# Kernel tuning notes

Measured on AMD Instinct MI355X. Metric: run time of the kernel, lower is better.

The kernel has to match this reference:

```python
import jax, jax.numpy as jnp
import numpy as np

N = 50000      # nodes
E = 600000     # edges
D_IN = 128
D_HID = 128
D_OUT = 64
BN_EPS = 1e-5


def _linear(key, fan_in, fan_out):
    s = 1.0 / np.sqrt(fan_in)
    kw, kb = jax.random.split(key)
    W = jax.random.uniform(kw, (fan_in, fan_out), jnp.float32, -s, s)
    b = jax.random.uniform(kb, (fan_out,), jnp.float32, -s, s)
    return W, b


def setup_inputs() -> dict:
    key = jax.random.key(0)
    ks = jax.random.split(key, 6)
    x = jax.random.normal(ks[0], (N, D_IN), jnp.float32)
    edge_index = jax.random.randint(ks[1], (2, E), 0, N, dtype=jnp.int64)
    W1, b1 = _linear(ks[2], D_IN, D_HID)
    W2, b2 = _linear(ks[3], D_HID, D_HID)
    W3, b3 = _linear(ks[4], D_HID, D_OUT)
    g1 = jnp.ones((D_HID,), jnp.float32); be1 = jnp.zeros((D_HID,), jnp.float32)
    g2 = jnp.ones((D_HID,), jnp.float32); be2 = jnp.zeros((D_HID,), jnp.float32)
    return {"x": x, "edge_index": edge_index,
            "W1": W1, "b1": b1, "g1": g1, "be1": be1,
            "W2": W2, "b2": b2, "g2": g2, "be2": be2,
            "W3": W3, "b3": b3}


def _gin_conv(x, src, dst, W, b):
    # GIN aggregation: h_i = (1+eps)*x_i + sum_{j->i} x_j, eps=0, then linear
    agg = jax.ops.segment_sum(x[src], dst, num_segments=N)  # [N, d]
    return (agg + x) @ W + b


def _bn(x, gamma, beta):
    # BatchNorm1d in training mode: batch statistics over nodes
    m = x.mean(axis=0)
    v = x.var(axis=0)
    return (x - m) * jax.lax.rsqrt(v + BN_EPS) * gamma + beta


def reference(x, edge_index, W1, b1, g1, be1, W2, b2, g2, be2, W3, b3):
    src, dst = edge_index[0], edge_index[1]
    h = jax.nn.relu(_bn(_gin_conv(x, src, dst, W1, b1), g1, be1))
    h = jax.nn.relu(_bn(_gin_conv(h, src, dst, W2, b2), g2, be2))
    h = _gin_conv(h, src, dst, W3, b3)
    return jax.nn.log_softmax(h, axis=-1)
```

## Files before the change

kernel.cpp:

```cpp
#include <hip/hip_runtime.h>

#define BN_EPS 1e-5f

typedef __attribute__((ext_vector_type(8))) __bf16 bf16x8;
typedef __attribute__((ext_vector_type(4))) float f32x4;

__device__ __forceinline__ unsigned short f2bf(float f) {
    unsigned int u = __float_as_uint(f);
    u = (u + 0x7fffu + ((u >> 16) & 1u)) >> 16;
    return (unsigned short)u;
}
__device__ __forceinline__ float bfLo(unsigned int w) { return __uint_as_float(w << 16); }
__device__ __forceinline__ float bfHi(unsigned int w) { return __uint_as_float(w & 0xffff0000u); }


__global__ void hist_kernel(const int* __restrict__ dst, int* __restrict__ deg, int E) {
    int e = blockIdx.x * blockDim.x + threadIdx.x;
    if (e < E) atomicAdd(&deg[dst[e]], 1);
}

__global__ void scan_block(const int* __restrict__ deg, int* __restrict__ incl,
                           int* __restrict__ bsum, int N) {
    __shared__ int s[256];
    int i = blockIdx.x * 256 + threadIdx.x;
    int v = (i < N) ? deg[i] : 0;
    s[threadIdx.x] = v;
    __syncthreads();
#pragma unroll
    for (int off = 1; off < 256; off <<= 1) {
        int t = (threadIdx.x >= off) ? s[threadIdx.x - off] : 0;
        __syncthreads();
        s[threadIdx.x] += t;
        __syncthreads();
    }
    if (i < N) incl[i] = s[threadIdx.x];
    if (threadIdx.x == 255) bsum[blockIdx.x] = s[255];
}

__global__ void scan_top(int* __restrict__ bsum, int nb) {
    __shared__ int s[256];
    int v = (threadIdx.x < nb) ? bsum[threadIdx.x] : 0;
    s[threadIdx.x] = v;
    __syncthreads();
#pragma unroll
    for (int off = 1; off < 256; off <<= 1) {
        int t = (threadIdx.x >= off) ? s[threadIdx.x - off] : 0;
        __syncthreads();
        s[threadIdx.x] += t;
        __syncthreads();
    }
    if (threadIdx.x < nb) bsum[threadIdx.x] = s[threadIdx.x] - v;
}

__global__ void finalize_rowptr(const int* __restrict__ deg, const int* __restrict__ incl,
                                const int* __restrict__ boff, int* __restrict__ rowptr,
                                int* __restrict__ pos, int N, int E) {
    int i = blockIdx.x * 256 + threadIdx.x;
    if (i < N) {
        int r = incl[i] - deg[i] + boff[i >> 8];
        rowptr[i] = r;
        pos[i] = r;
    }
    if (i == 0) rowptr[N] = E;
}

__global__ void fill_kernel(const int* __restrict__ src, const int* __restrict__ dst,
                            int* __restrict__ pos, int* __restrict__ col, int E) {
    int e = blockIdx.x * blockDim.x + threadIdx.x;
    if (e < E) {
        int slot = atomicAdd(&pos[dst[e]], 1);
        col[slot] = src[e];
    }
}

__global__ void convert_and_prep(const float* __restrict__ x, unsigned short* __restrict__ hb,
                                 int total4,
                                 const float* __restrict__ W1, const float* __restrict__ W2,
                                 const float* __restrict__ W3,
                                 unsigned short* __restrict__ w1s, unsigned short* __restrict__ w2s,
                                 unsigned short* __restrict__ w3s) {
    int tid0 = blockIdx.x * blockDim.x + threadIdx.x;
    if (tid0 < 40960) {
        int idx = tid0;
        const float* W; unsigned short* O; int NOUT;
        if (idx < 16384)      { W = W1; O = w1s; NOUT = 128; }
        else if (idx < 32768) { W = W2; O = w2s; NOUT = 128; idx -= 16384; }
        else                  { W = W3; O = w3s; NOUT = 64;  idx -= 32768; }
        int j = idx & 7;
        int l = (idx >> 3) & 63;
        int q = (idx >> 9) & 3;
        int ct = idx >> 11;
        int k = q * 32 + ((l >> 4) & 3) * 8 + j;
        int c = ct * 16 + (l & 15);
        O[idx] = f2bf(W[(size_t)k * NOUT + c]);
    }
    int stride = gridDim.x * blockDim.x;
    for (int i = tid0; i < total4; i += stride) {
        float4 v = reinterpret_cast<const float4*>(x)[i];
        ushort4 o;
        o.x = f2bf(v.x); o.y = f2bf(v.y); o.z = f2bf(v.z); o.w = f2bf(v.w);
        reinterpret_cast<ushort4*>(hb)[i] = o;
    }
}

__global__ void gather_agg_bf(const unsigned short* __restrict__ h,
                              const int* __restrict__ rowptr, const int* __restrict__ col,
                              unsigned short* __restrict__ agg, int N) {
    int t = blockIdx.x * blockDim.x + threadIdx.x;
    int node = t >> 4;
    if (node >= N) return;
    int part = (t & 15) * 8;
    const int beg = rowptr[node], end = rowptr[node + 1];

    float acc[8];
    {
        uint4 sv = *reinterpret_cast<const uint4*>(h + (size_t)node * 128 + part);
        acc[0] = bfLo(sv.x); acc[1] = bfHi(sv.x);
        acc[2] = bfLo(sv.y); acc[3] = bfHi(sv.y);
        acc[4] = bfLo(sv.z); acc[5] = bfHi(sv.z);
        acc[6] = bfLo(sv.w); acc[7] = bfHi(sv.w);
    }
    int e = beg;
    for (; e + 1 < end; e += 2) {
        int s0 = col[e], s1 = col[e + 1];
        uint4 v0 = *reinterpret_cast<const uint4*>(h + (size_t)s0 * 128 + part);
        uint4 v1 = *reinterpret_cast<const uint4*>(h + (size_t)s1 * 128 + part);
        acc[0] += bfLo(v0.x) + bfLo(v1.x); acc[1] += bfHi(v0.x) + bfHi(v1.x);
        acc[2] += bfLo(v0.y) + bfLo(v1.y); acc[3] += bfHi(v0.y) + bfHi(v1.y);
        acc[4] += bfLo(v0.z) + bfLo(v1.z); acc[5] += bfHi(v0.z) + bfHi(v1.z);
        acc[6] += bfLo(v0.w) + bfLo(v1.w); acc[7] += bfHi(v0.w) + bfHi(v1.w);
    }
    if (e < end) {
        uint4 v0 = *reinterpret_cast<const uint4*>(h + (size_t)col[e] * 128 + part);
        acc[0] += bfLo(v0.x); acc[1] += bfHi(v0.x);
        acc[2] += bfLo(v0.y); acc[3] += bfHi(v0.y);
        acc[4] += bfLo(v0.z); acc[5] += bfHi(v0.z);
        acc[6] += bfLo(v0.w); acc[7] += bfHi(v0.w);
    }
    uint4 o;
    o.x = (unsigned int)f2bf(acc[0]) | ((unsigned int)f2bf(acc[1]) << 16);
    o.y = (unsigned int)f2bf(acc[2]) | ((unsigned int)f2bf(acc[3]) << 16);
    o.z = (unsigned int)f2bf(acc[4]) | ((unsigned int)f2bf(acc[5]) << 16);
    o.w = (unsigned int)f2bf(acc[6]) | ((unsigned int)f2bf(acc[7]) << 16);
    *reinterpret_cast<uint4*>(agg + (size_t)node * 128 + part) = o;
}

__global__ __launch_bounds__(256) void gemm128_stats(const unsigned short* __restrict__ A,
                                                     const unsigned short* __restrict__ Wsw,
                                                     const float* __restrict__ bias,
                                                     float* __restrict__ out,
                                                     float* __restrict__ sumsPad,
                                                     float* __restrict__ sqsPad, int N) {
    __shared__ float red[2][4][128];
    const int lane = threadIdx.x & 63;
    const int w = threadIdx.x >> 6;
    const int r0 = blockIdx.x * 64 + w * 16;
    int arow = r0 + (lane & 15);
    if (arow >= N) arow = N - 1;
    const int kb = lane >> 4;
    const unsigned short* ap = A + (size_t)arow * 128 + kb * 8;

    bf16x8 a[4];
#pragma unroll
    for (int q = 0; q < 4; ++q) a[q] = *reinterpret_cast<const bf16x8*>(ap + q * 32);

    f32x4 acc[8];
#pragma unroll
    for (int ct = 0; ct < 8; ++ct) acc[ct] = (f32x4){0.f, 0.f, 0.f, 0.f};

    const bf16x8* wp = reinterpret_cast<const bf16x8*>(Wsw) + lane;
#pragma unroll
    for (int ct = 0; ct < 8; ++ct)
#pragma unroll
        for (int q = 0; q < 4; ++q)
            acc[ct] = __builtin_amdgcn_mfma_f32_16x16x32_bf16(a[q], wp[(ct * 4 + q) * 64],
                                                              acc[ct], 0, 0, 0);

    const int crow0 = r0 + (lane >> 4) * 4;
    const int ccol = lane & 15;
#pragma unroll
    for (int ct = 0; ct < 8; ++ct) {
        int c = ct * 16 + ccol;
        float bv = bias[c];
        float s = 0.f, qq = 0.f;
#pragma unroll
        for (int j = 0; j < 4; ++j) {
            int r = crow0 + j;
            if (r < N) {
                float o = acc[ct][j] + bv;
                out[(size_t)r * 128 + c] = o;
                s += o; qq += o * o;
            }
        }
        s += __shfl_xor(s, 16); s += __shfl_xor(s, 32);
        qq += __shfl_xor(qq, 16); qq += __shfl_xor(qq, 32);
        if (lane < 16) { red[0][w][c] = s; red[1][w][c] = qq; }
    }
    __syncthreads();
    int tid = threadIdx.x;
    if (tid < 128) {
        float S = red[0][0][tid] + red[0][1][tid] + red[0][2][tid] + red[0][3][tid];
        atomicAdd(&sumsPad[tid * 16], S);
    } else {
        int c = tid - 128;
        float Q = red[1][0][c] + red[1][1][c] + red[1][2][c] + red[1][3][c];
        atomicAdd(&sqsPad[c * 16], Q);
    }
}

__global__ __launch_bounds__(256) void gemm64_lsm(const unsigned short* __restrict__ A,
                                                  const unsigned short* __restrict__ Wsw,
                                                  const float* __restrict__ bias,
                                                  float* __restrict__ out, int N) {
    const int lane = threadIdx.x & 63;
    const int w = threadIdx.x >> 6;
    const int r0 = blockIdx.x * 64 + w * 16;
    int arow = r0 + (lane & 15);
    if (arow >= N) arow = N - 1;
    const int kb = lane >> 4;
    const unsigned short* ap = A + (size_t)arow * 128 + kb * 8;

    bf16x8 a[4];
#pragma unroll
    for (int q = 0; q < 4; ++q) a[q] = *reinterpret_cast<const bf16x8*>(ap + q * 32);

    f32x4 acc[4];
#pragma unroll
    for (int ct = 0; ct < 4; ++ct) acc[ct] = (f32x4){0.f, 0.f, 0.f, 0.f};

    const bf16x8* wp = reinterpret_cast<const bf16x8*>(Wsw) + lane;
#pragma unroll
    for (int ct = 0; ct < 4; ++ct)
#pragma unroll
        for (int q = 0; q < 4; ++q)
            acc[ct] = __builtin_amdgcn_mfma_f32_16x16x32_bf16(a[q], wp[(ct * 4 + q) * 64],
                                                              acc[ct], 0, 0, 0);

    const int crow0 = r0 + (lane >> 4) * 4;
    const int ccol = lane & 15;
    float bv[4];
#pragma unroll
    for (int ct = 0; ct < 4; ++ct) bv[ct] = bias[ct * 16 + ccol];

#pragma unroll
    for (int j = 0; j < 4; ++j) {
        float o0 = acc[0][j] + bv[0], o1 = acc[1][j] + bv[1];
        float o2 = acc[2][j] + bv[2], o3 = acc[3][j] + bv[3];
        float m = fmaxf(fmaxf(o0, o1), fmaxf(o2, o3));
#pragma unroll
        for (int off = 1; off < 16; off <<= 1) m = fmaxf(m, __shfl_xor(m, off));
        float s = __expf(o0 - m) + __expf(o1 - m) + __expf(o2 - m) + __expf(o3 - m);
#pragma unroll
        for (int off = 1; off < 16; off <<= 1) s += __shfl_xor(s, off);
        float ml = m + __logf(s);
        int r = crow0 + j;
        if (r < N) {
            float* op = out + (size_t)r * 64 + ccol;
            op[0]  = o0 - ml;
            op[16] = o1 - ml;
            op[32] = o2 - ml;
            op[48] = o3 - ml;
        }
    }
}

__global__ void bn_relu_bf16(const float* __restrict__ t, const float* __restrict__ sumsPad,
                             const float* __restrict__ sqsPad, const float* __restrict__ g,
                             const float* __restrict__ be, unsigned short* __restrict__ h,
                             int total4, float invN) {
    const int idx0 = blockIdx.x * blockDim.x + threadIdx.x;
    const int stride = gridDim.x * blockDim.x;
    const int col = (idx0 * 4) & 127;
    float a4[4], c4[4];
#pragma unroll
    for (int k = 0; k < 4; ++k) {
        int c = col + k;
        float m = sumsPad[c * 16] * invN;
        float v = sqsPad[c * 16] * invN - m * m;
        float ai = g[c] * rsqrtf(v + BN_EPS);
        a4[k] = ai;
        c4[k] = be[c] - m * ai;
    }
    for (int idx = idx0; idx < total4; idx += stride) {
        float4 v = reinterpret_cast<const float4*>(t)[idx];
        ushort4 o;
        o.x = f2bf(fmaxf(fmaf(v.x, a4[0], c4[0]), 0.f));
        o.y = f2bf(fmaxf(fmaf(v.y, a4[1], c4[1]), 0.f));
        o.z = f2bf(fmaxf(fmaf(v.z, a4[2], c4[2]), 0.f));
        o.w = f2bf(fmaxf(fmaf(v.w, a4[3], c4[3]), 0.f));
        reinterpret_cast<ushort4*>(h)[idx] = o;
    }
}

extern "C" void kernel_launch(void* const* d_in, const int* in_sizes, int n_in,
                              void* d_out, int out_size, void* d_ws, size_t ws_size,
                              hipStream_t stream) {
    const float* x   = (const float*)d_in[0];
    const int*   ei  = (const int*)d_in[1];
    const float* W1  = (const float*)d_in[2];
    const float* b1  = (const float*)d_in[3];
    const float* g1  = (const float*)d_in[4];
    const float* be1 = (const float*)d_in[5];
    const float* W2  = (const float*)d_in[6];
    const float* b2  = (const float*)d_in[7];
    const float* g2  = (const float*)d_in[8];
    const float* be2 = (const float*)d_in[9];
    const float* W3  = (const float*)d_in[10];
    const float* b3  = (const float*)d_in[11];

    const int N = in_sizes[0] / 128;
    const int E = in_sizes[1] / 2;
    const int* src = ei;
    const int* dst = ei + E;

    float* f1           = (float*)d_ws;
    unsigned short* hb  = (unsigned short*)(f1 + (size_t)N * 128);
    unsigned short* agb = hb + (size_t)N * 128;
    unsigned short* w1s = agb + (size_t)N * 128;
    unsigned short* w2s = w1s + 16384;
    unsigned short* w3s = w2s + 16384;
    float* statsPad = (float*)(w3s + 8192);
    float* sums1 = statsPad;
    float* sqs1  = statsPad + 2048;
    float* sums2 = statsPad + 4096;
    float* sqs2  = statsPad + 6144;
    int* deg    = (int*)(statsPad + 8192);
    int* pos    = deg + N;
    int* rowptr = pos + N;
    int* bsum   = rowptr + N + 1;
    int* colidx = bsum + 256;

    const int nChunks = (N + 255) / 256;
    const int eBlocks = (E + 255) / 256;
    const int gemmBlocks = (N + 63) / 64;
    const int gatherBlocks = (N * 16 + 255) / 256;
    const int total4 = N * 128 / 4;

    hipMemsetAsync(statsPad, 0, 8192 * sizeof(float) + (size_t)N * sizeof(int), stream);

    convert_and_prep<<<2048, 256, 0, stream>>>(x, hb, total4, W1, W2, W3, w1s, w2s, w3s);
    hist_kernel<<<eBlocks, 256, 0, stream>>>(dst, deg, E);
    scan_block<<<nChunks, 256, 0, stream>>>(deg, pos, bsum, N);
    scan_top<<<1, 256, 0, stream>>>(bsum, nChunks);
    finalize_rowptr<<<nChunks, 256, 0, stream>>>(deg, pos, bsum, rowptr, pos, N, E);
    fill_kernel<<<eBlocks, 256, 0, stream>>>(src, dst, pos, colidx, E);

    gather_agg_bf<<<gatherBlocks, 256, 0, stream>>>(hb, rowptr, colidx, agb, N);
    gemm128_stats<<<gemmBlocks, 256, 0, stream>>>(agb, w1s, b1, f1, sums1, sqs1, N);
    bn_relu_bf16<<<2048, 256, 0, stream>>>(f1, sums1, sqs1, g1, be1, hb, total4, 1.0f / N);

    gather_agg_bf<<<gatherBlocks, 256, 0, stream>>>(hb, rowptr, colidx, agb, N);
    gemm128_stats<<<gemmBlocks, 256, 0, stream>>>(agb, w2s, b2, f1, sums2, sqs2, N);
    bn_relu_bf16<<<2048, 256, 0, stream>>>(f1, sums2, sqs2, g2, be2, hb, total4, 1.0f / N);

    gather_agg_bf<<<gatherBlocks, 256, 0, stream>>>(hb, rowptr, colidx, agb, N);
    gemm64_lsm<<<gemmBlocks, 256, 0, stream>>>(agb, w3s, b3, (float*)d_out, N);
}
```

Baseline: 258.3 us.

## Fuse BN+ReLU into gather, store GEMM output as bf16, degree-sort nodes

The GEMM epilogue now writes pre-BN activations as bf16 instead of fp32, and the standalone bn_relu pass is removed. BN scale/shift and ReLU are instead applied on the fly to every gathered neighbor row inside a new gather_bn_agg kernel. Nodes are also bucketed by degree via a histogram and permutation so that the 16-lane groups in a wavefront handle nodes of similar degree, which reduces divergence. The trade-off is redundant BN arithmetic per edge, plus rounding to bf16 before the normalization is applied.

```diff
diff --git a/kernel.cpp b/kernel.cpp
--- a/kernel.cpp
+++ b/kernel.cpp
@@ -20,12 +20,15 @@
 }
 
 __global__ void scan_block(const int* __restrict__ deg, int* __restrict__ incl,
-                           int* __restrict__ bsum, int N) {
+                           int* __restrict__ bsum, int* __restrict__ bhist, int N) {
     __shared__ int s[256];
+    __shared__ int bh[64];
     int i = blockIdx.x * 256 + threadIdx.x;
     int v = (i < N) ? deg[i] : 0;
     s[threadIdx.x] = v;
+    if (threadIdx.x < 64) bh[threadIdx.x] = 0;
     __syncthreads();
+    if (i < N) atomicAdd(&bh[v < 63 ? v : 63], 1);
 #pragma unroll
     for (int off = 1; off < 256; off <<= 1) {
         int t = (threadIdx.x >= off) ? s[threadIdx.x - off] : 0;
@@ -35,9 +38,11 @@
     }
     if (i < N) incl[i] = s[threadIdx.x];
     if (threadIdx.x == 255) bsum[blockIdx.x] = s[255];
-}
-
-__global__ void scan_top(int* __restrict__ bsum, int nb) {
+    if (threadIdx.x < 64 && bh[threadIdx.x] > 0) atomicAdd(&bhist[threadIdx.x], bh[threadIdx.x]);
+}
+
+__global__ void scan_top(int* __restrict__ bsum, int nb,
+                         const int* __restrict__ bhist, int* __restrict__ bpos) {
     __shared__ int s[256];
     int v = (threadIdx.x < nb) ? bsum[threadIdx.x] : 0;
     s[threadIdx.x] = v;
@@ -50,16 +55,30 @@
         __syncthreads();
     }
     if (threadIdx.x < nb) bsum[threadIdx.x] = s[threadIdx.x] - v;
+    if (threadIdx.x < 64) {
+        int bv = bhist[threadIdx.x];
+        int inc = bv;
+#pragma unroll
+        for (int off = 1; off < 64; off <<= 1) {
+            int t = __shfl_up(inc, off);
+            if ((threadIdx.x & 63) >= off) inc += t;
+        }
+        bpos[threadIdx.x] = inc - bv;
+    }
 }
 
 __global__ void finalize_rowptr(const int* __restrict__ deg, const int* __restrict__ incl,
                                 const int* __restrict__ boff, int* __restrict__ rowptr,
-                                int* __restrict__ pos, int N, int E) {
+                                int* __restrict__ pos, int* __restrict__ bpos,
+                                int* __restrict__ perm, int N, int E) {
     int i = blockIdx.x * 256 + threadIdx.x;
     if (i < N) {
-        int r = incl[i] - deg[i] + boff[i >> 8];
+        int d = deg[i];
+        int r = incl[i] - d + boff[i >> 8];
         rowptr[i] = r;
         pos[i] = r;
+        int slot = atomicAdd(&bpos[d < 63 ? d : 63], 1);
+        perm[slot] = i;
     }
     if (i == 0) rowptr[N] = E;
 }
@@ -105,10 +124,12 @@
 
 __global__ void gather_agg_bf(const unsigned short* __restrict__ h,
                               const int* __restrict__ rowptr, const int* __restrict__ col,
+                              const int* __restrict__ perm,
                               unsigned short* __restrict__ agg, int N) {
     int t = blockIdx.x * blockDim.x + threadIdx.x;
-    int node = t >> 4;
-    if (node >= N) return;
+    int ni = t >> 4;
+    if (ni >= N) return;
+    int node = perm[ni];
     int part = (t & 15) * 8;
     const int beg = rowptr[node], end = rowptr[node + 1];
 
@@ -145,10 +166,65 @@
     *reinterpret_cast<uint4*>(agg + (size_t)node * 128 + part) = o;
 }
 
+__global__ void gather_bn_agg(const unsigned short* __restrict__ raw,
+                              const float* __restrict__ sumsPad, const float* __restrict__ sqsPad,
+                              const float* __restrict__ g, const float* __restrict__ be,
+                              const int* __restrict__ rowptr, const int* __restrict__ col,
+                              const int* __restrict__ perm,
+                              unsigned short* __restrict__ agg, int N, float invN) {
+    int t = blockIdx.x * blockDim.x + threadIdx.x;
+    int ni = t >> 4;
+    if (ni >= N) return;
+    int node = perm[ni];
+    int part = (t & 15) * 8;
+    float a8[8], c8[8];
+#pragma unroll
+    for (int k = 0; k < 8; ++k) {
+        int c = part + k;
+        float m = sumsPad[c * 16] * invN;
+        float v = sqsPad[c * 16] * invN - m * m;
+        float ai = g[c] * rsqrtf(v + BN_EPS);
+        a8[k] = ai;
+        c8[k] = be[c] - m * ai;
+    }
+    const int beg = rowptr[node], end = rowptr[node + 1];
+    float acc[8];
+    {
+        uint4 sv = *reinterpret_cast<const uint4*>(raw + (size_t)node * 128 + part);
+        float e0 = bfLo(sv.x), e1 = bfHi(sv.x), e2 = bfLo(sv.y), e3 = bfHi(sv.y);
+        float e4 = bfLo(sv.z), e5 = bfHi(sv.z), e6 = bfLo(sv.w), e7 = bfHi(sv.w);
+        acc[0] = fmaxf(fmaf(e0, a8[0], c8[0]), 0.f);
+        acc[1] = fmaxf(fmaf(e1, a8[1], c8[1]), 0.f);
+        acc[2] = fmaxf(fmaf(e2, a8[2], c8[2]), 0.f);
+        acc[3] = fmaxf(fmaf(e3, a8[3], c8[3]), 0.f);
+        acc[4] = fmaxf(fmaf(e4, a8[4], c8[4]), 0.f);
+        acc[5] = fmaxf(fmaf(e5, a8[5], c8[5]), 0.f);
+        acc[6] = fmaxf(fmaf(e6, a8[6], c8[6]), 0.f);
+        acc[7] = fmaxf(fmaf(e7, a8[7], c8[7]), 0.f);
+    }
+    for (int e = beg; e < end; ++e) {
+        uint4 v0 = *reinterpret_cast<const uint4*>(raw + (size_t)col[e] * 128 + part);
+        acc[0] += fmaxf(fmaf(bfLo(v0.x), a8[0], c8[0]), 0.f);
+        acc[1] += fmaxf(fmaf(bfHi(v0.x), a8[1], c8[1]), 0.f);
+        acc[2] += fmaxf(fmaf(bfLo(v0.y), a8[2], c8[2]), 0.f);
+        acc[3] += fmaxf(fmaf(bfHi(v0.y), a8[3], c8[3]), 0.f);
+        acc[4] += fmaxf(fmaf(bfLo(v0.z), a8[4], c8[4]), 0.f);
+        acc[5] += fmaxf(fmaf(bfHi(v0.z), a8[5], c8[5]), 0.f);
+        acc[6] += fmaxf(fmaf(bfLo(v0.w), a8[6], c8[6]), 0.f);
+        acc[7] += fmaxf(fmaf(bfHi(v0.w), a8[7], c8[7]), 0.f);
+    }
+    uint4 o;
+    o.x = (unsigned int)f2bf(acc[0]) | ((unsigned int)f2bf(acc[1]) << 16);
+    o.y = (unsigned int)f2bf(acc[2]) | ((unsigned int)f2bf(acc[3]) << 16);
+    o.z = (unsigned int)f2bf(acc[4]) | ((unsigned int)f2bf(acc[5]) << 16);
+    o.w = (unsigned int)f2bf(acc[6]) | ((unsigned int)f2bf(acc[7]) << 16);
+    *reinterpret_cast<uint4*>(agg + (size_t)node * 128 + part) = o;
+}
+
 __global__ __launch_bounds__(256) void gemm128_stats(const unsigned short* __restrict__ A,
                                                      const unsigned short* __restrict__ Wsw,
                                                      const float* __restrict__ bias,
-                                                     float* __restrict__ out,
+                                                     unsigned short* __restrict__ outb,
                                                      float* __restrict__ sumsPad,
                                                      float* __restrict__ sqsPad, int N) {
     __shared__ float red[2][4][128];
@@ -188,7 +264,7 @@
             int r = crow0 + j;
             if (r < N) {
                 float o = acc[ct][j] + bv;
-                out[(size_t)r * 128 + c] = o;
+                outb[(size_t)r * 128 + c] = f2bf(o);
                 s += o; qq += o * o;
             }
         }
@@ -261,34 +337,6 @@
             op[32] = o2 - ml;
             op[48] = o3 - ml;
         }
-    }
-}
-
-__global__ void bn_relu_bf16(const float* __restrict__ t, const float* __restrict__ sumsPad,
-                             const float* __restrict__ sqsPad, const float* __restrict__ g,
-                             const float* __restrict__ be, unsigned short* __restrict__ h,
-                             int total4, float invN) {
-    const int idx0 = blockIdx.x * blockDim.x + threadIdx.x;
-    const int stride = gridDim.x * blockDim.x;
-    const int col = (idx0 * 4) & 127;
-    float a4[4], c4[4];
-#pragma unroll
-    for (int k = 0; k < 4; ++k) {
-        int c = col + k;
-        float m = sumsPad[c * 16] * invN;
-        float v = sqsPad[c * 16] * invN - m * m;
-        float ai = g[c] * rsqrtf(v + BN_EPS);
-        a4[k] = ai;
-        c4[k] = be[c] - m * ai;
-    }
-    for (int idx = idx0; idx < total4; idx += stride) {
-        float4 v = reinterpret_cast<const float4*>(t)[idx];
-        ushort4 o;
-        o.x = f2bf(fmaxf(fmaf(v.x, a4[0], c4[0]), 0.f));
-        o.y = f2bf(fmaxf(fmaf(v.y, a4[1], c4[1]), 0.f));
-        o.z = f2bf(fmaxf(fmaf(v.z, a4[2], c4[2]), 0.f));
-        o.w = f2bf(fmaxf(fmaf(v.w, a4[3], c4[3]), 0.f));
-        reinterpret_cast<ushort4*>(h)[idx] = o;
     }
 }
 
@@ -313,46 +361,50 @@
     const int* src = ei;
     const int* dst = ei + E;
 
-    float* f1           = (float*)d_ws;
-    unsigned short* hb  = (unsigned short*)(f1 + (size_t)N * 128);
-    unsigned short* agb = hb + (size_t)N * 128;
-    unsigned short* w1s = agb + (size_t)N * 128;
-    unsigned short* w2s = w1s + 16384;
-    unsigned short* w3s = w2s + 16384;
-    float* statsPad = (float*)(w3s + 8192);
+    float* statsPad = (float*)d_ws;
     float* sums1 = statsPad;
     float* sqs1  = statsPad + 2048;
     float* sums2 = statsPad + 4096;
     float* sqs2  = statsPad + 6144;
     int* deg    = (int*)(statsPad + 8192);
-    int* pos    = deg + N;
+    int* bhist  = deg + N;
+    int* bpos   = bhist + 64;
+    int* pos    = bpos + 64;
     int* rowptr = pos + N;
     int* bsum   = rowptr + N + 1;
-    int* colidx = bsum + 256;
+    int* perm   = bsum + 256;
+    int* colidx = perm + N;
+    unsigned short* hb   = (unsigned short*)(colidx + E);
+    unsigned short* rawb = hb + (size_t)N * 128;
+    unsigned short* agb  = rawb + (size_t)N * 128;
+    unsigned short* w1s  = agb + (size_t)N * 128;
+    unsigned short* w2s  = w1s + 16384;
+    unsigned short* w3s  = w2s + 16384;
 
     const int nChunks = (N + 255) / 256;
     const int eBlocks = (E + 255) / 256;
     const int gemmBlocks = (N + 63) / 64;
     const int gatherBlocks = (N * 16 + 255) / 256;
     const int total4 = N * 128 / 4;
-
-    hipMemsetAsync(statsPad, 0, 8192 * sizeof(float) + (size_t)N * sizeof(int), stream);
+    const float invN = 1.0f / N;
+
+    hipMemsetAsync(statsPad, 0, 8192 * sizeof(float) + ((size_t)N + 128) * sizeof(int), stream);
 
     convert_and_prep<<<2048, 256, 0, stream>>>(x, hb, total4, W1, W2, W3, w1s, w2s, w3s);
     hist_kernel<<<eBlocks, 256, 0, stream>>>(dst, deg, E);
-    scan_block<<<nChunks, 256, 0, stream>>>(deg, pos, bsum, N);
-    scan_top<<<1, 256, 0, stream>>>(bsum, nChunks);
-    finalize_rowptr<<<nChunks, 256, 0, stream>>>(deg, pos, bsum, rowptr, pos, N, E);
+    scan_block<<<nChunks, 256, 0, stream>>>(deg, pos, bsum, bhist, N);
+    scan_top<<<1, 256, 0, stream>>>(bsum, nChunks, bhist, bpos);
+    finalize_rowptr<<<nChunks, 256, 0, stream>>>(deg, pos, bsum, rowptr, pos, bpos, perm, N, E);
     fill_kernel<<<eBlocks, 256, 0, stream>>>(src, dst, pos, colidx, E);
 
-    gather_agg_bf<<<gatherBlocks, 256, 0, stream>>>(hb, rowptr, colidx, agb, N);
-    gemm128_stats<<<gemmBlocks, 256, 0, stream>>>(agb, w1s, b1, f1, sums1, sqs1, N);
-    bn_relu_bf16<<<2048, 256, 0, stream>>>(f1, sums1, sqs1, g1, be1, hb, total4, 1.0f / N);
-
-    gather_agg_bf<<<gatherBlocks, 256, 0, stream>>>(hb, rowptr, colidx, agb, N);
-    gemm128_stats<<<gemmBlocks, 256, 0, stream>>>(agb, w2s, b2, f1, sums2, sqs2, N);
-    bn_relu_bf16<<<2048, 256, 0, stream>>>(f1, sums2, sqs2, g2, be2, hb, total4, 1.0f / N);
-
-    gather_agg_bf<<<gatherBlocks, 256, 0, stream>>>(hb, rowptr, colidx, agb, N);
+    gather_agg_bf<<<gatherBlocks, 256, 0, stream>>>(hb, rowptr, colidx, perm, agb, N);
+    gemm128_stats<<<gemmBlocks, 256, 0, stream>>>(agb, w1s, b1, rawb, sums1, sqs1, N);
+
+    gather_bn_agg<<<gatherBlocks, 256, 0, stream>>>(rawb, sums1, sqs1, g1, be1, rowptr, colidx,
+                                                    perm, agb, N, invN);
+    gemm128_stats<<<gemmBlocks, 256, 0, stream>>>(agb, w2s, b2, rawb, sums2, sqs2, N);
+
+    gather_bn_agg<<<gatherBlocks, 256, 0, stream>>>(rawb, sums2, sqs2, g2, be2, rowptr, colidx,
+                                                    perm, agb, N, invN);
     gemm64_lsm<<<gemmBlocks, 256, 0, stream>>>(agb, w3s, b3, (float*)d_out, N);
 }
```

Result: slower. 458.0 us (+77.3%).

## Fuse BN+ReLU into gathers, reorder last layer as GEMM-then-gather with fused log-softmax

Applied to the files above, without the earlier changes.

Removes the standalone BN+ReLU passes by applying the normalisation inside the next layer's gather, and stores the GEMM pre-activation output in bf16 instead of fp32. The last layer is reordered to multiply by W3 first (BN applied in the GEMM's A-load) and then aggregate 64-wide rows, fusing bias and log-softmax into that gather. This cuts memory traffic and kernel launches, at the cost of recomputing BN+ReLU per gathered edge and adding bf16 rounding of the pre-BN activations. The gather loops are also unrolled by four.

```diff
diff --git a/kernel.cpp b/kernel.cpp
--- a/kernel.cpp
+++ b/kernel.cpp
@@ -12,6 +12,23 @@
 }
 __device__ __forceinline__ float bfLo(unsigned int w) { return __uint_as_float(w << 16); }
 __device__ __forceinline__ float bfHi(unsigned int w) { return __uint_as_float(w & 0xffff0000u); }
+
+__device__ __forceinline__ void accRow(float* acc, uint4 v) {
+    acc[0] += bfLo(v.x); acc[1] += bfHi(v.x);
+    acc[2] += bfLo(v.y); acc[3] += bfHi(v.y);
+    acc[4] += bfLo(v.z); acc[5] += bfHi(v.z);
+    acc[6] += bfLo(v.w); acc[7] += bfHi(v.w);
+}
+__device__ __forceinline__ void accRowBN(float* acc, uint4 v, const float* a8, const float* c8) {
+    acc[0] += fmaxf(fmaf(bfLo(v.x), a8[0], c8[0]), 0.f);
+    acc[1] += fmaxf(fmaf(bfHi(v.x), a8[1], c8[1]), 0.f);
+    acc[2] += fmaxf(fmaf(bfLo(v.y), a8[2], c8[2]), 0.f);
+    acc[3] += fmaxf(fmaf(bfHi(v.y), a8[3], c8[3]), 0.f);
+    acc[4] += fmaxf(fmaf(bfLo(v.z), a8[4], c8[4]), 0.f);
+    acc[5] += fmaxf(fmaf(bfHi(v.z), a8[5], c8[5]), 0.f);
+    acc[6] += fmaxf(fmaf(bfLo(v.w), a8[6], c8[6]), 0.f);
+    acc[7] += fmaxf(fmaf(bfHi(v.w), a8[7], c8[7]), 0.f);
+}
 
 
 __global__ void hist_kernel(const int* __restrict__ dst, int* __restrict__ deg, int E) {
@@ -110,33 +127,29 @@
     int node = t >> 4;
     if (node >= N) return;
     int part = (t & 15) * 8;
+    const unsigned short* hp = h + part;
     const int beg = rowptr[node], end = rowptr[node + 1];
 
     float acc[8];
     {
-        uint4 sv = *reinterpret_cast<const uint4*>(h + (size_t)node * 128 + part);
+        uint4 sv = *reinterpret_cast<const uint4*>(hp + (size_t)node * 128);
         acc[0] = bfLo(sv.x); acc[1] = bfHi(sv.x);
         acc[2] = bfLo(sv.y); acc[3] = bfHi(sv.y);
         acc[4] = bfLo(sv.z); acc[5] = bfHi(sv.z);
         acc[6] = bfLo(sv.w); acc[7] = bfHi(sv.w);
     }
     int e = beg;
-    for (; e + 1 < end; e += 2) {
-        int s0 = col[e], s1 = col[e + 1];
-        uint4 v0 = *reinterpret_cast<const uint4*>(h + (size_t)s0 * 128 + part);
-        uint4 v1 = *reinterpret_cast<const uint4*>(h + (size_t)s1 * 128 + part);
-        acc[0] += bfLo(v0.x) + bfLo(v1.x); acc[1] += bfHi(v0.x) + bfHi(v1.x);
-        acc[2] += bfLo(v0.y) + bfLo(v1.y); acc[3] += bfHi(v0.y) + bfHi(v1.y);
-        acc[4] += bfLo(v0.z) + bfLo(v1.z); acc[5] += bfHi(v0.z) + bfHi(v1.z);
-        acc[6] += bfLo(v0.w) + bfLo(v1.w); acc[7] += bfHi(v0.w) + bfHi(v1.w);
-    }
-    if (e < end) {
-        uint4 v0 = *reinterpret_cast<const uint4*>(h + (size_t)col[e] * 128 + part);
-        acc[0] += bfLo(v0.x); acc[1] += bfHi(v0.x);
-        acc[2] += bfLo(v0.y); acc[3] += bfHi(v0.y);
-        acc[4] += bfLo(v0.z); acc[5] += bfHi(v0.z);
-        acc[6] += bfLo(v0.w); acc[7] += bfHi(v0.w);
-    }
+    for (; e + 3 < end; e += 4) {
+        int s0 = col[e], s1 = col[e + 1], s2 = col[e + 2], s3 = col[e + 3];
+        uint4 v0 = *reinterpret_cast<const uint4*>(hp + (size_t)s0 * 128);
+        uint4 v1 = *reinterpret_cast<const uint4*>(hp + (size_t)s1 * 128);
+        uint4 v2 = *reinterpret_cast<const uint4*>(hp + (size_t)s2 * 128);
+        uint4 v3 = *reinterpret_cast<const uint4*>(hp + (size_t)s3 * 128);
+        accRow(acc, v0); accRow(acc, v1); accRow(acc, v2); accRow(acc, v3);
+    }
+    for (; e < end; ++e)
+        accRow(acc, *reinterpret_cast<const uint4*>(hp + (size_t)col[e] * 128));
+
     uint4 o;
     o.x = (unsigned int)f2bf(acc[0]) | ((unsigned int)f2bf(acc[1]) << 16);
     o.y = (unsigned int)f2bf(acc[2]) | ((unsigned int)f2bf(acc[3]) << 16);
@@ -145,10 +158,54 @@
     *reinterpret_cast<uint4*>(agg + (size_t)node * 128 + part) = o;
 }
 
+__global__ void gather_bn_agg(const unsigned short* __restrict__ raw,
+                              const float* __restrict__ sumsPad, const float* __restrict__ sqsPad,
+                              const float* __restrict__ g, const float* __restrict__ be,
+                              const int* __restrict__ rowptr, const int* __restrict__ col,
+                              unsigned short* __restrict__ agg, int N, float invN) {
+    int t = blockIdx.x * blockDim.x + threadIdx.x;
+    int node = t >> 4;
+    if (node >= N) return;
+    int part = (t & 15) * 8;
+    const unsigned short* rp = raw + part;
+    float a8[8], c8[8];
+#pragma unroll
+    for (int k = 0; k < 8; ++k) {
+        int c = part + k;
+        float m = sumsPad[c * 16] * invN;
+        float v = sqsPad[c * 16] * invN - m * m;
+        float ai = g[c] * rsqrtf(v + BN_EPS);
+        a8[k] = ai;
+        c8[k] = be[c] - m * ai;
+    }
+    const int beg = rowptr[node], end = rowptr[node + 1];
+    float acc[8] = {0.f, 0.f, 0.f, 0.f, 0.f, 0.f, 0.f, 0.f};
+    accRowBN(acc, *reinterpret_cast<const uint4*>(rp + (size_t)node * 128), a8, c8);
+    int e = beg;
+    for (; e + 3 < end; e += 4) {
+        int s0 = col[e], s1 = col[e + 1], s2 = col[e + 2], s3 = col[e + 3];
+        uint4 v0 = *reinterpret_cast<const uint4*>(rp + (size_t)s0 * 128);
+        uint4 v1 = *reinterpret_cast<const uint4*>(rp + (size_t)s1 * 128);
+        uint4 v2 = *reinterpret_cast<const uint4*>(rp + (size_t)s2 * 128);
+        uint4 v3 = *reinterpret_cast<const uint4*>(rp + (size_t)s3 * 128);
+        accRowBN(acc, v0, a8, c8); accRowBN(acc, v1, a8, c8);
+        accRowBN(acc, v2, a8, c8); accRowBN(acc, v3, a8, c8);
+    }
+    for (; e < end; ++e)
+        accRowBN(acc, *reinterpret_cast<const uint4*>(rp + (size_t)col[e] * 128), a8, c8);
+
+    uint4 o;
+    o.x = (unsigned int)f2bf(acc[0]) | ((unsigned int)f2bf(acc[1]) << 16);
+    o.y = (unsigned int)f2bf(acc[2]) | ((unsigned int)f2bf(acc[3]) << 16);
+    o.z = (unsigned int)f2bf(acc[4]) | ((unsigned int)f2bf(acc[5]) << 16);
+    o.w = (unsigned int)f2bf(acc[6]) | ((unsigned int)f2bf(acc[7]) << 16);
+    *reinterpret_cast<uint4*>(agg + (size_t)node * 128 + part) = o;
+}
+
 __global__ __launch_bounds__(256) void gemm128_stats(const unsigned short* __restrict__ A,
                                                      const unsigned short* __restrict__ Wsw,
                                                      const float* __restrict__ bias,
-                                                     float* __restrict__ out,
+                                                     unsigned short* __restrict__ outb,
                                                      float* __restrict__ sumsPad,
                                                      float* __restrict__ sqsPad, int N) {
     __shared__ float red[2][4][128];
@@ -188,7 +245,7 @@
             int r = crow0 + j;
             if (r < N) {
                 float o = acc[ct][j] + bv;
-                out[(size_t)r * 128 + c] = o;
+                outb[(size_t)r * 128 + c] = f2bf(o);
                 s += o; qq += o * o;
             }
         }
@@ -208,21 +265,49 @@
     }
 }
 
-__global__ __launch_bounds__(256) void gemm64_lsm(const unsigned short* __restrict__ A,
-                                                  const unsigned short* __restrict__ Wsw,
-                                                  const float* __restrict__ bias,
-                                                  float* __restrict__ out, int N) {
+__global__ __launch_bounds__(256) void gemm64_bn(const unsigned short* __restrict__ raw,
+                                                 const float* __restrict__ sumsPad,
+                                                 const float* __restrict__ sqsPad,
+                                                 const float* __restrict__ g,
+                                                 const float* __restrict__ be,
+                                                 const unsigned short* __restrict__ Wsw,
+                                                 unsigned short* __restrict__ M, int N,
+                                                 float invN) {
     const int lane = threadIdx.x & 63;
     const int w = threadIdx.x >> 6;
     const int r0 = blockIdx.x * 64 + w * 16;
     int arow = r0 + (lane & 15);
     if (arow >= N) arow = N - 1;
     const int kb = lane >> 4;
-    const unsigned short* ap = A + (size_t)arow * 128 + kb * 8;
+    const unsigned short* ap = raw + (size_t)arow * 128 + kb * 8;
 
     bf16x8 a[4];
 #pragma unroll
-    for (int q = 0; q < 4; ++q) a[q] = *reinterpret_cast<const bf16x8*>(ap + q * 32);
+    for (int q = 0; q < 4; ++q) {
+        uint4 rv = *reinterpret_cast<const uint4*>(ap + q * 32);
+        float e0 = bfLo(rv.x), e1 = bfHi(rv.x), e2 = bfLo(rv.y), e3 = bfHi(rv.y);
+        float e4 = bfLo(rv.z), e5 = bfHi(rv.z), e6 = bfLo(rv.w), e7 = bfHi(rv.w);
+        float hh[8] = {e0, e1, e2, e3, e4, e5, e6, e7};
+        uint4 hp;
+        unsigned int pk[4];
+#pragma unroll
+        for (int p = 0; p < 4; ++p) {
+            unsigned int lohi[2];
+#pragma unroll
+            for (int hl = 0; hl < 2; ++hl) {
+                int j = p * 2 + hl;
+                int c = q * 32 + kb * 8 + j;
+                float mcol = sumsPad[c * 16] * invN;
+                float var = sqsPad[c * 16] * invN - mcol * mcol;
+                float ai = g[c] * rsqrtf(var + BN_EPS);
+                float ci = be[c] - mcol * ai;
+                lohi[hl] = f2bf(fmaxf(fmaf(hh[j], ai, ci), 0.f));
+            }
+            pk[p] = lohi[0] | (lohi[1] << 16);
+        }
+        hp.x = pk[0]; hp.y = pk[1]; hp.z = pk[2]; hp.w = pk[3];
+        a[q] = *reinterpret_cast<bf16x8*>(&hp);
+    }
 
     f32x4 acc[4];
 #pragma unroll
@@ -238,58 +323,68 @@
 
     const int crow0 = r0 + (lane >> 4) * 4;
     const int ccol = lane & 15;
-    float bv[4];
-#pragma unroll
-    for (int ct = 0; ct < 4; ++ct) bv[ct] = bias[ct * 16 + ccol];
-
-#pragma unroll
-    for (int j = 0; j < 4; ++j) {
-        float o0 = acc[0][j] + bv[0], o1 = acc[1][j] + bv[1];
-        float o2 = acc[2][j] + bv[2], o3 = acc[3][j] + bv[3];
-        float m = fmaxf(fmaxf(o0, o1), fmaxf(o2, o3));
-#pragma unroll
-        for (int off = 1; off < 16; off <<= 1) m = fmaxf(m, __shfl_xor(m, off));
-        float s = __expf(o0 - m) + __expf(o1 - m) + __expf(o2 - m) + __expf(o3 - m);
-#pragma unroll
-        for (int off = 1; off < 16; off <<= 1) s += __shfl_xor(s, off);
-        float ml = m + __logf(s);
-        int r = crow0 + j;
-        if (r < N) {
-            float* op = out + (size_t)r * 64 + ccol;
-            op[0]  = o0 - ml;
-            op[16] = o1 - ml;
-            op[32] = o2 - ml;
-            op[48] = o3 - ml;
+#pragma unroll
+    for (int ct = 0; ct < 4; ++ct) {
+        int c = ct * 16 + ccol;
+#pragma unroll
+        for (int j = 0; j < 4; ++j) {
+            int r = crow0 + j;
+            if (r < N) M[(size_t)r * 64 + c] = f2bf(acc[ct][j]);
         }
     }
 }
 
-__global__ void bn_relu_bf16(const float* __restrict__ t, const float* __restrict__ sumsPad,
-                             const float* __restrict__ sqsPad, const float* __restrict__ g,
-                             const float* __restrict__ be, unsigned short* __restrict__ h,
-                             int total4, float invN) {
-    const int idx0 = blockIdx.x * blockDim.x + threadIdx.x;
-    const int stride = gridDim.x * blockDim.x;
-    const int col = (idx0 * 4) & 127;
-    float a4[4], c4[4];
-#pragma unroll
-    for (int k = 0; k < 4; ++k) {
-        int c = col + k;
-        float m = sumsPad[c * 16] * invN;
-        float v = sqsPad[c * 16] * invN - m * m;
-        float ai = g[c] * rsqrtf(v + BN_EPS);
-        a4[k] = ai;
-        c4[k] = be[c] - m * ai;
-    }
-    for (int idx = idx0; idx < total4; idx += stride) {
-        float4 v = reinterpret_cast<const float4*>(t)[idx];
-        ushort4 o;
-        o.x = f2bf(fmaxf(fmaf(v.x, a4[0], c4[0]), 0.f));
-        o.y = f2bf(fmaxf(fmaf(v.y, a4[1], c4[1]), 0.f));
-        o.z = f2bf(fmaxf(fmaf(v.z, a4[2], c4[2]), 0.f));
-        o.w = f2bf(fmaxf(fmaf(v.w, a4[3], c4[3]), 0.f));
-        reinterpret_cast<ushort4*>(h)[idx] = o;
-    }
+__global__ void gather64_lsm(const unsigned short* __restrict__ M,
+                             const int* __restrict__ rowptr, const int* __restrict__ col,
+                             const float* __restrict__ bias, float* __restrict__ out, int N) {
+    int t = blockIdx.x * blockDim.x + threadIdx.x;
+    int node = t >> 3;
+    if (node >= N) return;
+    int part = (t & 7) * 8;
+    const unsigned short* mp = M + part;
+    const int beg = rowptr[node], end = rowptr[node + 1];
+
+    float acc[8];
+    {
+        uint4 sv = *reinterpret_cast<const uint4*>(mp + (size_t)node * 64);
+        acc[0] = bfLo(sv.x); acc[1] = bfHi(sv.x);
+        acc[2] = bfLo(sv.y); acc[3] = bfHi(sv.y);
+        acc[4] = bfLo(sv.z); acc[5] = bfHi(sv.z);
+        acc[6] = bfLo(sv.w); acc[7] = bfHi(sv.w);
+    }
+    int e = beg;
+    for (; e + 3 < end; e += 4) {
+        int s0 = col[e], s1 = col[e + 1], s2 = col[e + 2], s3 = col[e + 3];
+        uint4 v0 = *reinterpret_cast<const uint4*>(mp + (size_t)s0 * 64);
+        uint4 v1 = *reinterpret_cast<const uint4*>(mp + (size_t)s1 * 64);
+        uint4 v2 = *reinterpret_cast<const uint4*>(mp + (size_t)s2 * 64);
+        uint4 v3 = *reinterpret_cast<const uint4*>(mp + (size_t)s3 * 64);
+        accRow(acc, v0); accRow(acc, v1); accRow(acc, v2); accRow(acc, v3);
+    }
+    for (; e < end; ++e)
+        accRow(acc, *reinterpret_cast<const uint4*>(mp + (size_t)col[e] * 64));
+
+#pragma unroll
+    for (int k = 0; k < 8; ++k) acc[k] += bias[part + k];
+
+    float m = acc[0];
+#pragma unroll
+    for (int k = 1; k < 8; ++k) m = fmaxf(m, acc[k]);
+#pragma unroll
+    for (int off = 1; off < 8; off <<= 1) m = fmaxf(m, __shfl_xor(m, off));
+    float s = 0.f;
+#pragma unroll
+    for (int k = 0; k < 8; ++k) s += __expf(acc[k] - m);
+#pragma unroll
+    for (int off = 1; off < 8; off <<= 1) s += __shfl_xor(s, off);
+    float ml = m + __logf(s);
+
+    float4 o0, o1;
+    o0.x = acc[0] - ml; o0.y = acc[1] - ml; o0.z = acc[2] - ml; o0.w = acc[3] - ml;
+    o1.x = acc[4] - ml; o1.y = acc[5] - ml; o1.z = acc[6] - ml; o1.w = acc[7] - ml;
+    float* op = out + (size_t)node * 64 + part;
+    *reinterpret_cast<float4*>(op) = o0;
+    *reinterpret_cast<float4*>(op + 4) = o1;
 }
 
 extern "C" void kernel_launch(void* const* d_in, const int* in_sizes, int n_in,
@@ -313,13 +408,7 @@
     const int* src = ei;
     const int* dst = ei + E;
 
-    float* f1           = (float*)d_ws;
-    unsigned short* hb  = (unsigned short*)(f1 + (size_t)N * 128);
-    unsigned short* agb = hb + (size_t)N * 128;
-    unsigned short* w1s = agb + (size_t)N * 128;
-    unsigned short* w2s = w1s + 16384;
-    unsigned short* w3s = w2s + 16384;
-    float* statsPad = (float*)(w3s + 8192);
+    float* statsPad = (float*)d_ws;
     float* sums1 = statsPad;
     float* sqs1  = statsPad + 2048;
     float* sums2 = statsPad + 4096;
@@ -329,12 +418,21 @@
     int* rowptr = pos + N;
     int* bsum   = rowptr + N + 1;
     int* colidx = bsum + 256;
+    unsigned short* hb   = (unsigned short*)(colidx + E);
+    unsigned short* rawb = hb + (size_t)N * 128;
+    unsigned short* agb  = rawb + (size_t)N * 128;
+    unsigned short* m3   = agb + (size_t)N * 128;
+    unsigned short* w1s  = m3 + (size_t)N * 64;
+    unsigned short* w2s  = w1s + 16384;
+    unsigned short* w3s  = w2s + 16384;
 
     const int nChunks = (N + 255) / 256;
     const int eBlocks = (E + 255) / 256;
     const int gemmBlocks = (N + 63) / 64;
     const int gatherBlocks = (N * 16 + 255) / 256;
+    const int gather64Blocks = (N * 8 + 255) / 256;
     const int total4 = N * 128 / 4;
+    const float invN = 1.0f / N;
 
     hipMemsetAsync(statsPad, 0, 8192 * sizeof(float) + (size_t)N * sizeof(int), stream);
 
@@ -346,13 +444,12 @@
     fill_kernel<<<eBlocks, 256, 0, stream>>>(src, dst, pos, colidx, E);
 
     gather_agg_bf<<<gatherBlocks, 256, 0, stream>>>(hb, rowptr, colidx, agb, N);
-    gemm128_stats<<<gemmBlocks, 256, 0, stream>>>(agb, w1s, b1, f1, sums1, sqs1, N);
-    bn_relu_bf16<<<2048, 256, 0, stream>>>(f1, sums1, sqs1, g1, be1, hb, total4, 1.0f / N);
-
-    gather_agg_bf<<<gatherBlocks, 256, 0, stream>>>(hb, rowptr, colidx, agb, N);
-    gemm128_stats<<<gemmBlocks, 256, 0, stream>>>(agb, w2s, b2, f1, sums2, sqs2, N);
-    bn_relu_bf16<<<2048, 256, 0, stream>>>(f1, sums2, sqs2, g2, be2, hb, total4, 1.0f / N);
-
-    gather_agg_bf<<<gatherBlocks, 256, 0, stream>>>(hb, rowptr, colidx, agb, N);
-    gemm64_lsm<<<gemmBlocks, 256, 0, stream>>>(agb, w3s, b3, (float*)d_out, N);
-}
+    gemm128_stats<<<gemmBlocks, 256, 0, stream>>>(agb, w1s, b1, rawb, sums1, sqs1, N);
+
+    gather_bn_agg<<<gatherBlocks, 256, 0, stream>>>(rawb, sums1, sqs1, g1, be1, rowptr, colidx,
+                                                    agb, N, invN);
+    gemm128_stats<<<gemmBlocks, 256, 0, stream>>>(agb, w2s, b2, rawb, sums2, sqs2, N);
+
+    gemm64_bn<<<gemmBlocks, 256, 0, stream>>>(rawb, sums2, sqs2, g2, be2, w3s, m3, N, invN);
+    gather64_lsm<<<gather64Blocks, 256, 0, stream>>>(m3, rowptr, colidx, b3, (float*)d_out, N);
+}
```

New measurement: 252.5 us. 1.02x faster.
